# Kernel optimization log

Measured on AMD Instinct MI355X. Metric: run time of the kernel, lower is better.

The kernel has to match this reference:

```python
import jax, jax.numpy as jnp
import numpy as np

NEG = -1000.0  # matches the -1000 masking used in the original module


def setup_inputs() -> dict:
    key = jax.random.key(0)
    k0, k1, k2 = jax.random.split(key, 3)
    B, L, T = 512, 512, 32
    S = T + 2  # states: 0 = START, 1..T = tags, T+1 = STOP
    word_tag_value = jax.random.normal(k0, (B, L, T), dtype=jnp.float32)
    # xavier_uniform-style init for the transition matrix, then mask per the original
    a = float(np.sqrt(6.0 / (S + S)))
    translation = jax.random.uniform(k1, (S, S), dtype=jnp.float32, minval=-a, maxval=a)
    translation = translation.at[:, 0].set(NEG)       # nothing transitions into START
    translation = translation.at[S - 1, :].set(NEG)   # nothing transitions out of STOP
    real_tag = jax.random.randint(k2, (B, L), 1, T + 1)  # tags in 1..T
    return {"word_tag_value": word_tag_value, "translation": translation,
            "real_tag": real_tag, "output_loss": 1}


def _score_path(word_tag_value, translation, real_tag, T):
    # sum of emissions at the gold tags (tags 1..T index emission column tag-1)
    emit = jnp.take_along_axis(word_tag_value, (real_tag - 1)[..., None], axis=2)[..., 0]  # [B, L]
    score_emit = emit.sum(axis=1)
    # sum of transitions along the gold path + START/STOP transitions
    score_trans = translation[real_tag[:, :-1], real_tag[:, 1:]].sum(axis=1)
    score_trans = score_trans + translation[0, real_tag[:, 0]] + translation[real_tag[:, -1], T + 1]
    return score_emit + score_trans  # [B]


def _score_total(word_tag_value, translation, T):
    # forward algorithm (logsumexp recursion) over S = T+2 states
    B, L, _ = word_tag_value.shape
    # pad emissions to S states; START/STOP get NEG emission mid-sequence
    obs = jnp.pad(word_tag_value, ((0, 0), (0, 0), (1, 1)), constant_values=NEG)  # [B, L, S]
    # initial alpha: emissions of step 0 at tag states, 0 at START/STOP (as in original)
    alpha0 = jnp.pad(word_tag_value[:, 0, :], ((0, 0), (1, 1)), constant_values=0.0)  # [B, S]

    def step(alpha, obs_t):
        # scores[prev, cur] = alpha[prev] + obs_t[cur] + translation[prev, cur]
        m = alpha[:, :, None] + obs_t[:, None, :] + translation[None, :, :]  # [B, S, S]
        return jax.nn.logsumexp(m, axis=1), None

    alpha_T, _ = jax.lax.scan(step, alpha0, jnp.swapaxes(obs, 0, 1)[1:])  # scan over L-1 steps
    return jax.nn.logsumexp(alpha_T, axis=1)  # [B]


def reference(word_tag_value, translation, real_tag, output_loss):
    T = word_tag_value.shape[-1]
    if output_loss:
        return _score_total(word_tag_value, translation, T) - _score_path(word_tag_value, translation, real_tag, T)
    return None
```

## Files before the change

### kernel.cpp

```cpp
#include <hip/hip_runtime.h>


#define F2  1.4426950408889634f
#define LN2 0.6931471805599453f

__global__ __launch_bounds__(64) void crf_kernel(
    const float* __restrict__ wtv,
    const float* __restrict__ trans,
    const int*   __restrict__ rtag,
    float* __restrict__ out)
{
    __shared__ __align__(16) float tlds[1156];
    __shared__ __align__(16) float alds[64];

    const int b = blockIdx.x;
    const int l = threadIdx.x;
    const int h = l >> 5;
    const int c = l & 31;

    for (int k = l; k < 1156; k += 64) tlds[k] = trans[k];
    __syncthreads();

    float tc[32];
    #pragma unroll
    for (int k = 0; k < 32; ++k) {
        float tv = h ? tlds[(c + 1) * 34 + (k + 1)]
                     : tlds[(k + 1) * 34 + (c + 1)];
        tc[k] = __builtin_exp2f(F2 * tv);
    }
    float accInit = h ? 0.0f : __builtin_exp2f(F2 * tlds[c + 1]);

    const float* wb = wtv + (size_t)b * (512 * 32);
    const int*   tb = rtag + (size_t)b * 512;

    int tagf = tb[l];
    int tagb = tb[448 + l];
    int tag0 = __builtin_amdgcn_readlane(tagf, 0);
    int ptf  = tag0;
    int pcb  = 33;

    float v0    = wb[c];
    float st    = h ? 1.0f : __builtin_exp2f(F2 * v0);
    float pathE = (!h && (c == tag0 - 1)) ? v0 : 0.0f;
    float pathT = h ? 0.0f : tlds[tag0];
    int scaleE  = 0;

    const int rowstride = h ? -32 : 32;
    float vn[8], vc[8], eo[8];
    {
        const float* p = wb + (h ? 511 * 32 : 32) + c;
        #pragma unroll
        for (int j = 0; j < 8; ++j) vn[j] = p[j * rowstride];
    }

    for (int t0 = 1; t0 <= 249; t0 += 8) {
        #pragma unroll
        for (int j = 0; j < 8; ++j) { vc[j] = vn[j]; eo[j] = __builtin_exp2f(F2 * vc[j]); }
        {
            int i8 = t0 + 8;
            int row8 = h ? (512 - i8) : i8;
            const float* p = wb + row8 * 32 + c;
            #pragma unroll
            for (int j = 0; j < 8; ++j) vn[j] = p[j * rowstride];
        }
        #pragma unroll
        for (int j = 0; j < 8; ++j) {
            const int i = t0 + j;
            if ((i & 63) == 0)                 tagf = tb[i + l];
            if (((i & 63) == 1) && (i != 1))   tagb = tb[((512 - i) & ~63) + l];
            int ctf = __builtin_amdgcn_readlane(tagf, i & 63);
            int ctb = __builtin_amdgcn_readlane(tagb, (512 - i) & 63);

            float wval = h ? st * eo[j] : st;
            alds[l] = wval;
            __builtin_amdgcn_wave_barrier();
            const float4* a4 = (const float4*)(alds + (h << 5));
            float a0 = accInit, a1 = 0.0f, a2 = 0.0f, a3 = 0.0f;
            accInit = 0.0f;
            #pragma unroll
            for (int k = 0; k < 8; ++k) {
                float4 x = a4[k];
                a0 += x.x * tc[4 * k + 0];
                a1 += x.y * tc[4 * k + 1];
                a2 += x.z * tc[4 * k + 2];
                a3 += x.w * tc[4 * k + 3];
            }
            __builtin_amdgcn_wave_barrier();
            float s  = (a0 + a1) + (a2 + a3);
            float ns = h ? s : s * eo[j];

            bool doUpd = (i != 256) || (h == 0);
            st = doUpd ? ns : st;

            int myct = h ? ctb : ctf;
            if ((c == myct - 1) && doUpd) pathE += vc[j];
            int af_ = ptf * 34 + ctf;
            int ab_ = ctb * 34 + pcb;
            float tvv = tlds[h ? ab_ : af_];
            pathT += doUpd ? tvv : 0.0f;
            ptf = ctf;
            if (i != 256) pcb = ctb;
        }
        float m = st;
        m = fmaxf(m, __shfl_xor(m, 1));
        m = fmaxf(m, __shfl_xor(m, 2));
        m = fmaxf(m, __shfl_xor(m, 4));
        m = fmaxf(m, __shfl_xor(m, 8));
        m = fmaxf(m, __shfl_xor(m, 16));
        int e = ((__float_as_int(m) >> 23) & 0xff) - 127;
        st *= __int_as_float((127 - e) << 23);
        scaleE += e;
    }

    float bo   = __shfl_xor(st, 32);
    float prod = st * bo;
    prod += __shfl_xor(prod, 1);
    prod += __shfl_xor(prod, 2);
    prod += __shfl_xor(prod, 4);
    prod += __shfl_xor(prod, 8);
    prod += __shfl_xor(prod, 16);
    int scTot = scaleE + __shfl_xor(scaleE, 32);
    float total = ((float)scTot + __builtin_log2f(prod)) * LN2;

    pathE += __shfl_xor(pathE, 1);
    pathE += __shfl_xor(pathE, 2);
    pathE += __shfl_xor(pathE, 4);
    pathE += __shfl_xor(pathE, 8);
    pathE += __shfl_xor(pathE, 16);
    pathE += __shfl_xor(pathE, 32);
    float pT = pathT + __shfl_xor(pathT, 32) + tlds[ptf * 34 + pcb];

    if (l == 0) out[b] = total - (pathE + pT);
}

extern "C" void kernel_launch(void* const* d_in, const int* in_sizes, int n_in,
                              void* d_out, int out_size, void* d_ws, size_t ws_size,
                              hipStream_t stream) {
    const float* wtv   = (const float*)d_in[0];
    const float* trans = (const float*)d_in[1];
    const int*   rtag  = (const int*)d_in[2];
    (void)in_sizes; (void)n_in; (void)d_ws; (void)ws_size; (void)out_size;
    float* out = (float*)d_out;
    crf_kernel<<<512, 64, 0, stream>>>(wtv, trans, rtag, out);
}
```

Measured before the change: 140.5 us.

## Split forward/backward CRF recursions into separate waves using readlane broadcast

Each block now uses two 64-lane waves, one for the forward and one for the backward alpha recursion, instead of packing both halves into one wave. The per-step LDS exchange is replaced by 32 readlane broadcasts into scalar registers, so the matvec runs without wave barriers or LDS traffic. Renormalisation now happens every step, taking the exponent of one broadcast value instead of a shuffle max reduction. Gold-path tags are prefetched in vector batches, and the two waves combine their results through LDS with a block sync. The cost is twice the threads per block, heavy SGPR/VGPR pressure from 32 broadcasts per step, and half of each wave's lanes doing duplicate work.

Result: slower. 162.5 us (+15.7%).

```diff
diff --git a/kernel.cpp b/kernel.cpp
--- a/kernel.cpp
+++ b/kernel.cpp
@@ -4,133 +4,163 @@
 #define F2  1.4426950408889634f
 #define LN2 0.6931471805599453f
 
-__global__ __launch_bounds__(64) void crf_kernel(
+__device__ __forceinline__ float rdlane(float v, int p) {
+    return __int_as_float(__builtin_amdgcn_readlane(__float_as_int(v), p));
+}
+
+__global__ __launch_bounds__(128) void crf_kernel(
     const float* __restrict__ wtv,
     const float* __restrict__ trans,
     const int*   __restrict__ rtag,
     float* __restrict__ out)
 {
     __shared__ __align__(16) float tlds[1156];
-    __shared__ __align__(16) float alds[64];
+    __shared__ float xv[64];
+    __shared__ float xs[2];
+    __shared__ int   xe[2];
 
-    const int b = blockIdx.x;
-    const int l = threadIdx.x;
-    const int h = l >> 5;
-    const int c = l & 31;
+    const int  b   = blockIdx.x;
+    const int  tid = threadIdx.x;
+    const int  h   = tid >> 6;
+    const bool isB = (h != 0);
+    const int  l   = tid & 63;
+    const int  c   = l & 31;
 
-    for (int k = l; k < 1156; k += 64) tlds[k] = trans[k];
+    for (int k = tid; k < 1156; k += 128) tlds[k] = trans[k];
     __syncthreads();
 
     float tc[32];
     #pragma unroll
-    for (int k = 0; k < 32; ++k) {
-        float tv = h ? tlds[(c + 1) * 34 + (k + 1)]
-                     : tlds[(k + 1) * 34 + (c + 1)];
-        tc[k] = __builtin_exp2f(F2 * tv);
+    for (int p = 0; p < 32; ++p) {
+        float tv = isB ? tlds[(c + 1) * 34 + (p + 1)]
+                       : tlds[(p + 1) * 34 + (c + 1)];
+        tc[p] = __builtin_exp2f(F2 * tv);
     }
-    float accInit = h ? 0.0f : __builtin_exp2f(F2 * tlds[c + 1]);
+    float accInitV = isB ? 0.0f : __builtin_exp2f(F2 * tlds[c + 1]);
 
     const float* wb = wtv + (size_t)b * (512 * 32);
     const int*   tb = rtag + (size_t)b * 512;
 
-    int tagf = tb[l];
-    int tagb = tb[448 + l];
-    int tag0 = __builtin_amdgcn_readlane(tagf, 0);
-    int ptf  = tag0;
-    int pcb  = 33;
+    const int rowstride = isB ? -32 : 32;
 
-    float v0    = wb[c];
-    float st    = h ? 1.0f : __builtin_exp2f(F2 * v0);
-    float pathE = (!h && (c == tag0 - 1)) ? v0 : 0.0f;
-    float pathT = h ? 0.0f : tlds[tag0];
-    int scaleE  = 0;
+    float v0   = wb[(isB ? 511 * 32 : 0) + c];
+    float pub0 = __builtin_exp2f(F2 * v0);
+    float su[32];
+    #pragma unroll
+    for (int p = 0; p < 32; ++p) su[p] = rdlane(pub0, p);
 
-    const int rowstride = h ? -32 : 32;
+    int scaleE = 0;
+    int kCur   = ((__float_as_int(su[0]) >> 23) & 0xff) - 127;
+
+    int  tb0   = tb[0];
+    int  pt    = isB ? 33 : tb0;
+    float pathT = isB ? 0.0f : tlds[tb0];
+    float pathE = (!isB && (c == tb0 - 1)) ? v0 : 0.0f;
+    float pv    = v0;
+
+    int ctg[8], ntg[8];
+    #pragma unroll
+    for (int j = 0; j < 8; ++j) ctg[j] = tb[isB ? (511 - j) : (1 + j)];
+
     float vn[8], vc[8], eo[8];
     {
-        const float* p = wb + (h ? 511 * 32 : 32) + c;
+        const float* p0 = wb + (isB ? 510 * 32 : 32) + c;
         #pragma unroll
-        for (int j = 0; j < 8; ++j) vn[j] = p[j * rowstride];
+        for (int j = 0; j < 8; ++j) vn[j] = p0[j * rowstride];
     }
 
+    float res = pub0, bKeep = 0.0f;
+    int   bScale = 0;
+
     for (int t0 = 1; t0 <= 249; t0 += 8) {
+        const bool last = (t0 == 249);
         #pragma unroll
         for (int j = 0; j < 8; ++j) { vc[j] = vn[j]; eo[j] = __builtin_exp2f(F2 * vc[j]); }
         {
-            int i8 = t0 + 8;
-            int row8 = h ? (512 - i8) : i8;
-            const float* p = wb + row8 * 32 + c;
+            int row8 = isB ? (511 - (t0 + 8)) : (t0 + 8);
+            const float* p0 = wb + row8 * 32 + c;
             #pragma unroll
-            for (int j = 0; j < 8; ++j) vn[j] = p[j * rowstride];
+            for (int j = 0; j < 8; ++j) vn[j] = p0[j * rowstride];
         }
+        {
+            #pragma unroll
+            for (int j = 0; j < 8; ++j) ntg[j] = tb[isB ? (504 - t0 - j) : (t0 + 8 + j)];
+        }
+        float ptv[8];
         #pragma unroll
         for (int j = 0; j < 8; ++j) {
-            const int i = t0 + j;
-            if ((i & 63) == 0)                 tagf = tb[i + l];
-            if (((i & 63) == 1) && (i != 1))   tagb = tb[((512 - i) & ~63) + l];
-            int ctf = __builtin_amdgcn_readlane(tagf, i & 63);
-            int ctb = __builtin_amdgcn_readlane(tagb, (512 - i) & 63);
+            int ct  = ctg[j];
+            int idx = isB ? (ct * 34 + pt) : (pt * 34 + ct);
+            ptv[j]  = tlds[idx];
+            pt      = ct;
+        }
+        float seedv = (t0 == 1) ? accInitV : 0.0f;
 
-            float wval = h ? st * eo[j] : st;
-            alds[l] = wval;
-            __builtin_amdgcn_wave_barrier();
-            const float4* a4 = (const float4*)(alds + (h << 5));
-            float a0 = accInit, a1 = 0.0f, a2 = 0.0f, a3 = 0.0f;
-            accInit = 0.0f;
+        #pragma unroll
+        for (int j = 0; j < 8; ++j) {
+            float a0 = 0.0f, a1 = 0.0f, a2 = 0.0f, a3 = 0.0f;
             #pragma unroll
-            for (int k = 0; k < 8; ++k) {
-                float4 x = a4[k];
-                a0 += x.x * tc[4 * k + 0];
-                a1 += x.y * tc[4 * k + 1];
-                a2 += x.z * tc[4 * k + 2];
-                a3 += x.w * tc[4 * k + 3];
+            for (int p = 0; p < 32; p += 4) {
+                a0 = fmaf(su[p + 0], tc[p + 0], a0);
+                a1 = fmaf(su[p + 1], tc[p + 1], a1);
+                a2 = fmaf(su[p + 2], tc[p + 2], a2);
+                a3 = fmaf(su[p + 3], tc[p + 3], a3);
             }
-            __builtin_amdgcn_wave_barrier();
-            float s  = (a0 + a1) + (a2 + a3);
-            float ns = h ? s : s * eo[j];
+            float s = (a0 + a1) + (a2 + a3);
+            if (j == 0) s += seedv;
 
-            bool doUpd = (i != 256) || (h == 0);
-            st = doUpd ? ns : st;
+            float sS = ldexpf(s, -kCur);
+            scaleE += kCur;
+            if (j == 6) {
+                if (last && isB) { bKeep = sS; bScale = scaleE; }
+            }
+            res = sS * eo[j];
 
-            int myct = h ? ctb : ctf;
-            if ((c == myct - 1) && doUpd) pathE += vc[j];
-            int af_ = ptf * 34 + ctf;
-            int ab_ = ctb * 34 + pcb;
-            float tvv = tlds[h ? ab_ : af_];
-            pathT += doUpd ? tvv : 0.0f;
-            ptf = ctf;
-            if (i != 256) pcb = ctb;
+            if (!(j == 7 && last && isB)) {
+                int   ct = ctg[j];
+                float em = isB ? pv : vc[j];
+                pathE += (c == ct - 1) ? em : 0.0f;
+            }
+            pv = vc[j];
+
+            if (!(j == 7 && last && isB)) {
+                #pragma unroll
+                for (int p = 0; p < 32; ++p) su[p] = rdlane(res, p);
+                kCur = ((__float_as_int(su[0]) >> 23) & 0xff) - 127;
+            }
         }
-        float m = st;
-        m = fmaxf(m, __shfl_xor(m, 1));
-        m = fmaxf(m, __shfl_xor(m, 2));
-        m = fmaxf(m, __shfl_xor(m, 4));
-        m = fmaxf(m, __shfl_xor(m, 8));
-        m = fmaxf(m, __shfl_xor(m, 16));
-        int e = ((__float_as_int(m) >> 23) & 0xff) - 127;
-        st *= __int_as_float((127 - e) << 23);
-        scaleE += e;
+        pathT += ((ptv[0] + ptv[1]) + (ptv[2] + ptv[3]))
+               + ((ptv[4] + ptv[5]) + (ptv[6] + ptv[7]));
+        #pragma unroll
+        for (int j = 0; j < 8; ++j) ctg[j] = ntg[j];
     }
 
-    float bo   = __shfl_xor(st, 32);
-    float prod = st * bo;
-    prod += __shfl_xor(prod, 1);
-    prod += __shfl_xor(prod, 2);
-    prod += __shfl_xor(prod, 4);
-    prod += __shfl_xor(prod, 8);
-    prod += __shfl_xor(prod, 16);
-    int scTot = scaleE + __shfl_xor(scaleE, 32);
-    float total = ((float)scTot + __builtin_log2f(prod)) * LN2;
+    float fin  = isB ? bKeep  : res;
+    int   finS = isB ? bScale : scaleE;
 
-    pathE += __shfl_xor(pathE, 1);
-    pathE += __shfl_xor(pathE, 2);
-    pathE += __shfl_xor(pathE, 4);
-    pathE += __shfl_xor(pathE, 8);
-    pathE += __shfl_xor(pathE, 16);
-    pathE += __shfl_xor(pathE, 32);
-    float pT = pathT + __shfl_xor(pathT, 32) + tlds[ptf * 34 + pcb];
+    float pe = pathE;
+    pe += __shfl_xor(pe, 1);
+    pe += __shfl_xor(pe, 2);
+    pe += __shfl_xor(pe, 4);
+    pe += __shfl_xor(pe, 8);
+    pe += __shfl_xor(pe, 16);
 
-    if (l == 0) out[b] = total - (pathE + pT);
+    if (l < 32) xv[h * 32 + c] = fin;
+    if (l == 0) { xs[h] = pe + pathT; xe[h] = finS; }
+    __syncthreads();
+
+    if (h == 0) {
+        float pr = xv[c] * xv[32 + c];
+        pr += __shfl_xor(pr, 1);
+        pr += __shfl_xor(pr, 2);
+        pr += __shfl_xor(pr, 4);
+        pr += __shfl_xor(pr, 8);
+        pr += __shfl_xor(pr, 16);
+        if (l == 0) {
+            float total = ((float)(xe[0] + xe[1]) + __builtin_log2f(pr)) * LN2;
+            out[b] = total - (xs[0] + xs[1]);
+        }
+    }
 }
 
 extern "C" void kernel_launch(void* const* d_in, const int* in_sizes, int n_in,
@@ -141,5 +171,5 @@
     const int*   rtag  = (const int*)d_in[2];
     (void)in_sizes; (void)n_in; (void)d_ws; (void)ws_size; (void)out_size;
     float* out = (float*)d_out;
-    crf_kernel<<<512, 64, 0, stream>>>(wtv, trans, rtag, out);
+    crf_kernel<<<512, 128, 0, stream>>>(wtv, trans, rtag, out);
 }
```

## Hoist gold-path scoring out of recurrence and rescale per step by leading element

Applied to the files above, without the earlier changes.

Gold-path emission and transition scores are now computed up front in parallel (8 positions per lane with vector tag loads) instead of being accumulated serially inside the forward/backward recurrence, removing the readlane, tag reload and LDS lookups from every step. The per-8-step max-shuffle renormalisation is replaced by per-step scaling with the exponent of the first alpha element, which drops the shuffle reductions but adds an exponent extraction and a multiply on every step. The i==256 special case is handled by saving the backward state one step early instead of branching inside the loop. Scaling by one element rather than the max could risk overflow or underflow if that element becomes tiny relative to the others.

Measured after the change: 155.7 us. +10.9%, slower.

```diff
diff --git a/kernel.cpp b/kernel.cpp
--- a/kernel.cpp
+++ b/kernel.cpp
@@ -18,119 +18,119 @@
     const int h = l >> 5;
     const int c = l & 31;
 
+    const float* wb = wtv + (size_t)b * (512 * 32);
+    const int*   tb = rtag + (size_t)b * 512;
+
     for (int k = l; k < 1156; k += 64) tlds[k] = trans[k];
     __syncthreads();
 
+    int tg[8];
+    {
+        const int4* tp = (const int4*)(tb + 8 * l);
+        int4 q0 = tp[0], q1 = tp[1];
+        tg[0] = q0.x; tg[1] = q0.y; tg[2] = q0.z; tg[3] = q0.w;
+        tg[4] = q1.x; tg[5] = q1.y; tg[6] = q1.z; tg[7] = q1.w;
+    }
+    int tExtra = tb[(l < 63) ? (8 * l + 8) : 511];
+    if (l == 63) tExtra = 33;
+    float path = 0.0f;
+    #pragma unroll
+    for (int j = 0; j < 8; ++j)
+        path += wb[(8 * l + j) * 32 + (tg[j] - 1)];
+    #pragma unroll
+    for (int j = 0; j < 8; ++j) {
+        int nxt = (j < 7) ? tg[j + 1] : tExtra;
+        path += tlds[tg[j] * 34 + nxt];
+    }
+    if (l == 0) path += tlds[tg[0]];
+
     float tc[32];
     #pragma unroll
-    for (int k = 0; k < 32; ++k) {
-        float tv = h ? tlds[(c + 1) * 34 + (k + 1)]
-                     : tlds[(k + 1) * 34 + (c + 1)];
-        tc[k] = __builtin_exp2f(F2 * tv);
+    for (int p = 0; p < 32; ++p) {
+        float tv = h ? tlds[(c + 1) * 34 + (p + 1)]
+                     : tlds[(p + 1) * 34 + (c + 1)];
+        tc[p] = __builtin_exp2f(F2 * tv);
     }
-    float accInit = h ? 0.0f : __builtin_exp2f(F2 * tlds[c + 1]);
+    float seed = h ? 0.0f : __builtin_exp2f(F2 * tlds[c + 1]);
 
-    const float* wb = wtv + (size_t)b * (512 * 32);
-    const int*   tb = rtag + (size_t)b * 512;
-
-    int tagf = tb[l];
-    int tagb = tb[448 + l];
-    int tag0 = __builtin_amdgcn_readlane(tagf, 0);
-    int ptf  = tag0;
-    int pcb  = 33;
-
-    float v0    = wb[c];
-    float st    = h ? 1.0f : __builtin_exp2f(F2 * v0);
-    float pathE = (!h && (c == tag0 - 1)) ? v0 : 0.0f;
-    float pathT = h ? 0.0f : tlds[tag0];
-    int scaleE  = 0;
+    float st = h ? 1.0f : __builtin_exp2f(F2 * wb[c]);
 
     const int rowstride = h ? -32 : 32;
-    float vn[8], vc[8], eo[8];
+    float vn[8];
     {
-        const float* p = wb + (h ? 511 * 32 : 32) + c;
+        const float* p0 = wb + (h ? 511 * 32 : 32) + c;
         #pragma unroll
-        for (int j = 0; j < 8; ++j) vn[j] = p[j * rowstride];
+        for (int j = 0; j < 8; ++j) vn[j] = p0[j * rowstride];
     }
 
+    int   scaleE = 0;
+    float bKeep  = 0.0f;
+    int   bScale = 0;
+
     for (int t0 = 1; t0 <= 249; t0 += 8) {
+        float eo[8];
         #pragma unroll
-        for (int j = 0; j < 8; ++j) { vc[j] = vn[j]; eo[j] = __builtin_exp2f(F2 * vc[j]); }
+        for (int j = 0; j < 8; ++j) eo[j] = __builtin_exp2f(F2 * vn[j]);
         {
-            int i8 = t0 + 8;
-            int row8 = h ? (512 - i8) : i8;
-            const float* p = wb + row8 * 32 + c;
+            const float* p0 = wb + (h ? (504 - t0) : (t0 + 8)) * 32 + c;
             #pragma unroll
-            for (int j = 0; j < 8; ++j) vn[j] = p[j * rowstride];
+            for (int j = 0; j < 8; ++j) vn[j] = p0[j * rowstride];
         }
+
         #pragma unroll
         for (int j = 0; j < 8; ++j) {
-            const int i = t0 + j;
-            if ((i & 63) == 0)                 tagf = tb[i + l];
-            if (((i & 63) == 1) && (i != 1))   tagb = tb[((512 - i) & ~63) + l];
-            int ctf = __builtin_amdgcn_readlane(tagf, i & 63);
-            int ctb = __builtin_amdgcn_readlane(tagb, (512 - i) & 63);
-
             float wval = h ? st * eo[j] : st;
             alds[l] = wval;
             __builtin_amdgcn_wave_barrier();
             const float4* a4 = (const float4*)(alds + (h << 5));
-            float a0 = accInit, a1 = 0.0f, a2 = 0.0f, a3 = 0.0f;
-            accInit = 0.0f;
-            #pragma unroll
-            for (int k = 0; k < 8; ++k) {
-                float4 x = a4[k];
-                a0 += x.x * tc[4 * k + 0];
-                a1 += x.y * tc[4 * k + 1];
-                a2 += x.z * tc[4 * k + 2];
-                a3 += x.w * tc[4 * k + 3];
-            }
+            float4 x0 = a4[0], x1 = a4[1], x2 = a4[2], x3 = a4[3];
+            float4 x4 = a4[4], x5 = a4[5], x6 = a4[6], x7 = a4[7];
             __builtin_amdgcn_wave_barrier();
-            float s  = (a0 + a1) + (a2 + a3);
-            float ns = h ? s : s * eo[j];
-
-            bool doUpd = (i != 256) || (h == 0);
-            st = doUpd ? ns : st;
-
-            int myct = h ? ctb : ctf;
-            if ((c == myct - 1) && doUpd) pathE += vc[j];
-            int af_ = ptf * 34 + ctf;
-            int ab_ = ctb * 34 + pcb;
-            float tvv = tlds[h ? ab_ : af_];
-            pathT += doUpd ? tvv : 0.0f;
-            ptf = ctf;
-            if (i != 256) pcb = ctb;
+            int k = ((__float_as_int(x0.x) >> 23) & 0xff) - 127;
+            float a0 = x0.x * tc[0],  a1 = x0.y * tc[1];
+            float a2 = x0.z * tc[2],  a3 = x0.w * tc[3];
+            a0 = fmaf(x1.x, tc[4],  a0); a1 = fmaf(x1.y, tc[5],  a1);
+            a2 = fmaf(x1.z, tc[6],  a2); a3 = fmaf(x1.w, tc[7],  a3);
+            a0 = fmaf(x2.x, tc[8],  a0); a1 = fmaf(x2.y, tc[9],  a1);
+            a2 = fmaf(x2.z, tc[10], a2); a3 = fmaf(x2.w, tc[11], a3);
+            a0 = fmaf(x3.x, tc[12], a0); a1 = fmaf(x3.y, tc[13], a1);
+            a2 = fmaf(x3.z, tc[14], a2); a3 = fmaf(x3.w, tc[15], a3);
+            a0 = fmaf(x4.x, tc[16], a0); a1 = fmaf(x4.y, tc[17], a1);
+            a2 = fmaf(x4.z, tc[18], a2); a3 = fmaf(x4.w, tc[19], a3);
+            a0 = fmaf(x5.x, tc[20], a0); a1 = fmaf(x5.y, tc[21], a1);
+            a2 = fmaf(x5.z, tc[22], a2); a3 = fmaf(x5.w, tc[23], a3);
+            a0 = fmaf(x6.x, tc[24], a0); a1 = fmaf(x6.y, tc[25], a1);
+            a2 = fmaf(x6.z, tc[26], a2); a3 = fmaf(x6.w, tc[27], a3);
+            a0 = fmaf(x7.x, tc[28], a0); a1 = fmaf(x7.y, tc[29], a1);
+            a2 = fmaf(x7.z, tc[30], a2); a3 = fmaf(x7.w, tc[31], a3);
+            float s = (a0 + a1) + (a2 + a3);
+            if (t0 == 1 && j == 0) s += seed;
+            float res = s * __int_as_float((127 - k) << 23);
+            st = h ? res : res * eo[j];
+            scaleE += k;
+            if (t0 == 249 && j == 6) { bKeep = st; bScale = scaleE; }
         }
-        float m = st;
-        m = fmaxf(m, __shfl_xor(m, 1));
-        m = fmaxf(m, __shfl_xor(m, 2));
-        m = fmaxf(m, __shfl_xor(m, 4));
-        m = fmaxf(m, __shfl_xor(m, 8));
-        m = fmaxf(m, __shfl_xor(m, 16));
-        int e = ((__float_as_int(m) >> 23) & 0xff) - 127;
-        st *= __int_as_float((127 - e) << 23);
-        scaleE += e;
     }
 
-    float bo   = __shfl_xor(st, 32);
+    float bo   = __shfl_xor(bKeep, 32);
     float prod = st * bo;
     prod += __shfl_xor(prod, 1);
     prod += __shfl_xor(prod, 2);
     prod += __shfl_xor(prod, 4);
     prod += __shfl_xor(prod, 8);
     prod += __shfl_xor(prod, 16);
-    int scTot = scaleE + __shfl_xor(scaleE, 32);
-    float total = ((float)scTot + __builtin_log2f(prod)) * LN2;
+    int scB = __shfl_xor(bScale, 32);
+    int scT = scaleE + scB;
 
-    pathE += __shfl_xor(pathE, 1);
-    pathE += __shfl_xor(pathE, 2);
-    pathE += __shfl_xor(pathE, 4);
-    pathE += __shfl_xor(pathE, 8);
-    pathE += __shfl_xor(pathE, 16);
-    pathE += __shfl_xor(pathE, 32);
-    float pT = pathT + __shfl_xor(pathT, 32) + tlds[ptf * 34 + pcb];
+    path += __shfl_xor(path, 1);
+    path += __shfl_xor(path, 2);
+    path += __shfl_xor(path, 4);
+    path += __shfl_xor(path, 8);
+    path += __shfl_xor(path, 16);
+    path += __shfl_xor(path, 32);
 
-    if (l == 0) out[b] = total - (pathE + pT);
+    if (l == 0)
+        out[b] = ((float)scT + __builtin_log2f(prod)) * LN2 - path;
 }
 
 extern "C" void kernel_launch(void* const* d_in, const int* in_sizes, int n_in,
```
